# Optimization experiments

Hardware: AMD Instinct MI355X
Metric: run time of the kernel (lower is better)

## Reference

```python
import jax, jax.numpy as jnp
import numpy as np

EPS = 1e-08
LEHMER_P = 1.0  # fixed_lehmer_param from init


def setup_inputs() -> dict:
    key = jax.random.key(0)
    x = jax.random.uniform(key, (2, 128, 7, 7), dtype=jnp.float32)
    return {"x": x}


def reference(x):
    B, C, H, W = x.shape
    F = H * W
    p = LEHMER_P

    # global max per batch element (max over channels and spatial)
    max_f = jnp.max(x.reshape(B, -1), axis=1)  # [B]
    x = jnp.nan_to_num(x / (max_f[:, None, None, None] + EPS))

    xf = x.reshape(B, C, F)  # [B, C, F]

    # pairwise outer product across channels and spatial positions
    # cross[b, m, n, i*F + j] = xf[b, m, i] * xf[b, n, j]
    cross = jnp.einsum('bmi,bnj->bmnij', xf, xf).reshape(B, C, C, F * F)

    numerators = jnp.nan_to_num(jnp.sum(jnp.nan_to_num((cross + EPS) ** (p + 1)), axis=3)) + EPS
    denominators = jnp.nan_to_num(jnp.sum(jnp.nan_to_num((cross + EPS) ** p), axis=3)) + EPS
    lehmer_numerators = jnp.nan_to_num(numerators / denominators) + EPS  # [B, C, C]

    a = jnp.abs(xf)
    num_den = jnp.nan_to_num(jnp.sum(jnp.nan_to_num((a + EPS) ** (p + 1)), axis=2)) + EPS  # [B, C]
    den_den = jnp.nan_to_num(jnp.sum(jnp.nan_to_num((a + EPS) ** p), axis=2)) + EPS  # [B, C]
    lehmer_denominator = jnp.nan_to_num(num_den / den_den) + EPS  # [B, C]

    # divide along the n (last) axis, matching torch unsqueeze(1)
    causality_maps = jnp.nan_to_num(lehmer_numerators / lehmer_denominator[:, None, :])
    return causality_maps
```

## Files before the change

kernel.cpp:

```cpp
#include <hip/hip_runtime.h>


constexpr float EPS = 1e-8f;
constexpr int B = 2, C = 128, F = 49;
constexpr int NIN  = B * C * F;
constexpr int HALF = NIN / 2;
constexpr int NOUT = B * C * C;
constexpr int BLK  = 1024;

__global__ __launch_bounds__(BLK)
void causality_kernel(const float* __restrict__ x, float* __restrict__ out) {
    __shared__ float sx[NIN];
    __shared__ float s1[B * C];
    __shared__ float s2[B * C];
    __shared__ float ld[B * C];
    __shared__ float rmax0[BLK / 64], rmax1[BLK / 64];
    __shared__ float bmax[B];

    const int tid  = threadIdx.x;
    const int lane = tid & 63;
    const int wid  = tid >> 6;

    float m0 = 0.f, m1 = 0.f;
    for (int i = tid; i < NIN; i += BLK) {
        float v = x[i];
        sx[i] = v;
        if (i < HALF) m0 = fmaxf(m0, v);
        else          m1 = fmaxf(m1, v);
    }
#pragma unroll
    for (int off = 32; off > 0; off >>= 1) {
        m0 = fmaxf(m0, __shfl_down(m0, off));
        m1 = fmaxf(m1, __shfl_down(m1, off));
    }
    if (lane == 0) { rmax0[wid] = m0; rmax1[wid] = m1; }
    __syncthreads();
    if (tid == 0) {
        float a = rmax0[0], b = rmax1[0];
        for (int w = 1; w < BLK / 64; ++w) {
            a = fmaxf(a, rmax0[w]);
            b = fmaxf(b, rmax1[w]);
        }
        bmax[0] = a; bmax[1] = b;
    }
    __syncthreads();

    {
        const int bc  = tid >> 2;
        const int sub = tid & 3;
        float a1 = 0.f, a2 = 0.f;
        const float* p = sx + bc * F;
        for (int k = sub; k < F; k += 4) {
            float v = p[k];
            a1 += v;
            a2 += v * v;
        }
        a1 += __shfl_down(a1, 2); a2 += __shfl_down(a2, 2);
        a1 += __shfl_down(a1, 1); a2 += __shfl_down(a2, 1);
        if (sub == 0) {
            const float inv = 1.f / (bmax[bc >> 7] + EPS);
            const float S1 = a1 * inv;
            const float S2 = a2 * inv * inv;
            s1[bc] = S1;
            s2[bc] = S2;
            const float nd = S2 + 2.f * EPS * S1 + (float)F * EPS * EPS + EPS;
            const float dd = S1 + (float)F * EPS + EPS;
            ld[bc] = nd / dd + EPS;
        }
    }
    __syncthreads();

    constexpr float F2 = (float)(F * F);
    for (int idx = tid; idx < NOUT; idx += BLK) {
        const int b  = idx >> 14;
        const int m  = (idx >> 7) & (C - 1);
        const int n  = idx & (C - 1);
        const int bm = (b << 7) | m;
        const int bn = (b << 7) | n;
        const float num = s2[bm] * s2[bn] + 2.f * EPS * (s1[bm] * s1[bn])
                          + F2 * EPS * EPS + EPS;
        const float den = s1[bm] * s1[bn] + F2 * EPS + EPS;
        const float ln  = num / den + EPS;
        out[idx] = ln / ld[bn];
    }
}

extern "C" void kernel_launch(void* const* d_in, const int* in_sizes, int n_in,
                              void* d_out, int out_size, void* d_ws, size_t ws_size,
                              hipStream_t stream) {
    const float* x = (const float*)d_in[0];
    float* out = (float*)d_out;
    causality_kernel<<<1, BLK, 0, stream>>>(x, out);
}
```

Baseline: 65.22 us.

## Spread output over 64 blocks with redundant per-block stats and fast reciprocals

Launches 64 blocks of 256 threads instead of a single 1024-thread block. Each block redundantly loads the whole input with float4 loads and computes the per-channel sums and the per-batch max, using one thread per channel. Each block then writes only its own slice of the 32K outputs. Divisions are replaced with hardware approximate reciprocals, which trades a little accuracy for fewer instructions, and every block repeats the input load and the reduction work.

```diff
diff --git a/kernel.cpp b/kernel.cpp
--- a/kernel.cpp
+++ b/kernel.cpp
@@ -4,84 +4,71 @@
 constexpr float EPS = 1e-8f;
 constexpr int B = 2, C = 128, F = 49;
 constexpr int NIN  = B * C * F;
-constexpr int HALF = NIN / 2;
+constexpr int N4   = NIN / 4;
+constexpr int BC   = B * C;
 constexpr int NOUT = B * C * C;
-constexpr int BLK  = 1024;
+constexpr int BLK  = 256;
+constexpr int GRID = 64;
 
 __global__ __launch_bounds__(BLK)
 void causality_kernel(const float* __restrict__ x, float* __restrict__ out) {
-    __shared__ float sx[NIN];
-    __shared__ float s1[B * C];
-    __shared__ float s2[B * C];
-    __shared__ float ld[B * C];
-    __shared__ float rmax0[BLK / 64], rmax1[BLK / 64];
-    __shared__ float bmax[B];
+    __shared__ __align__(16) float sx[NIN];
+    __shared__ float s1[BC], s2[BC], rld[BC];
+    __shared__ float wmax[BLK / 64];
 
     const int tid  = threadIdx.x;
     const int lane = tid & 63;
     const int wid  = tid >> 6;
 
-    float m0 = 0.f, m1 = 0.f;
-    for (int i = tid; i < NIN; i += BLK) {
-        float v = x[i];
-        sx[i] = v;
-        if (i < HALF) m0 = fmaxf(m0, v);
-        else          m1 = fmaxf(m1, v);
-    }
+    const float4* __restrict__ x4 = (const float4*)x;
+    float4* sx4 = (float4*)sx;
 #pragma unroll
-    for (int off = 32; off > 0; off >>= 1) {
-        m0 = fmaxf(m0, __shfl_down(m0, off));
-        m1 = fmaxf(m1, __shfl_down(m1, off));
-    }
-    if (lane == 0) { rmax0[wid] = m0; rmax1[wid] = m1; }
-    __syncthreads();
-    if (tid == 0) {
-        float a = rmax0[0], b = rmax1[0];
-        for (int w = 1; w < BLK / 64; ++w) {
-            a = fmaxf(a, rmax0[w]);
-            b = fmaxf(b, rmax1[w]);
-        }
-        bmax[0] = a; bmax[1] = b;
-    }
+    for (int i = 0; i < 12; ++i) sx4[tid + i * BLK] = x4[tid + i * BLK];
+    if (tid < N4 - 12 * BLK) sx4[tid + 12 * BLK] = x4[tid + 12 * BLK];
     __syncthreads();
 
-    {
-        const int bc  = tid >> 2;
-        const int sub = tid & 3;
-        float a1 = 0.f, a2 = 0.f;
-        const float* p = sx + bc * F;
-        for (int k = sub; k < F; k += 4) {
-            float v = p[k];
-            a1 += v;
-            a2 += v * v;
-        }
-        a1 += __shfl_down(a1, 2); a2 += __shfl_down(a2, 2);
-        a1 += __shfl_down(a1, 1); a2 += __shfl_down(a2, 1);
-        if (sub == 0) {
-            const float inv = 1.f / (bmax[bc >> 7] + EPS);
-            const float S1 = a1 * inv;
-            const float S2 = a2 * inv * inv;
-            s1[bc] = S1;
-            s2[bc] = S2;
-            const float nd = S2 + 2.f * EPS * S1 + (float)F * EPS * EPS + EPS;
-            const float dd = S1 + (float)F * EPS + EPS;
-            ld[bc] = nd / dd + EPS;
-        }
+    float a1 = 0.f, a2 = 0.f, mx = 0.f;
+    const float* p = sx + tid * F;
+#pragma unroll
+    for (int k = 0; k < F; ++k) {
+        float v = p[k];
+        a1 += v;
+        a2 += v * v;
+        mx = fmaxf(mx, v);
     }
+
+    float m = mx;
+#pragma unroll
+    for (int off = 32; off > 0; off >>= 1) m = fmaxf(m, __shfl_down(m, off));
+    if (lane == 0) wmax[wid] = m;
+    __syncthreads();
+    const int wb = (tid >> 7) << 1;
+    const float bmax = fmaxf(wmax[wb], wmax[wb + 1]);
+
+    const float inv = __builtin_amdgcn_rcpf(bmax + EPS);
+    const float S1 = a1 * inv;
+    const float S2 = a2 * inv * inv;
+    s1[tid] = S1;
+    s2[tid] = S2;
+    const float nd  = S2 + 2.f * EPS * S1 + (float)F * EPS * EPS + EPS;
+    const float dd  = S1 + (float)F * EPS + EPS;
+    const float ldv = nd * __builtin_amdgcn_rcpf(dd) + EPS;
+    rld[tid] = __builtin_amdgcn_rcpf(ldv);
     __syncthreads();
 
     constexpr float F2 = (float)(F * F);
-    for (int idx = tid; idx < NOUT; idx += BLK) {
-        const int b  = idx >> 14;
-        const int m  = (idx >> 7) & (C - 1);
-        const int n  = idx & (C - 1);
-        const int bm = (b << 7) | m;
-        const int bn = (b << 7) | n;
-        const float num = s2[bm] * s2[bn] + 2.f * EPS * (s1[bm] * s1[bn])
-                          + F2 * EPS * EPS + EPS;
-        const float den = s1[bm] * s1[bn] + F2 * EPS + EPS;
-        const float ln  = num / den + EPS;
-        out[idx] = ln / ld[bn];
+    const int base = blockIdx.x * (NOUT / GRID);
+#pragma unroll
+    for (int j = 0; j < NOUT / GRID / BLK; ++j) {
+        const int idx = base + tid + j * BLK;
+        const int bb  = (idx >> 14) << 7;
+        const int bm  = bb | ((idx >> 7) & (C - 1));
+        const int bn  = bb | (idx & (C - 1));
+        const float P   = s1[bm] * s1[bn];
+        const float num = s2[bm] * s2[bn] + 2.f * EPS * P + F2 * EPS * EPS + EPS;
+        const float den = P + F2 * EPS + EPS;
+        const float ln  = num * __builtin_amdgcn_rcpf(den) + EPS;
+        out[idx] = ln * rld[bn];
     }
 }
 
@@ -90,5 +77,5 @@
                               hipStream_t stream) {
     const float* x = (const float*)d_in[0];
     float* out = (float*)d_out;
-    causality_kernel<<<1, BLK, 0, stream>>>(x, out);
+    causality_kernel<<<GRID, BLK, 0, stream>>>(x, out);
 }
```

Result: faster. 53.17 us (-18.5%).
